# Optimization experiments

Hardware: AMD Instinct MI355X
Metric: run time of the kernel (lower is better)

## Reference

```python
import jax, jax.numpy as jnp
import numpy as np

N = 4096      # nnode
F = 128       # feature_dim
E = 64        # embed_dim
P_EDGE = 0.01 # edge probability (~41 avg degree)
NEG = -9e15
ALPHA = 0.2   # leaky relu slope


def _xavier(key, shape):
    lim = float(np.sqrt(6.0 / (shape[0] + shape[1])))
    return jax.random.uniform(key, shape, minval=-lim, maxval=lim, dtype=jnp.float32)


def setup_inputs() -> dict:
    key = jax.random.key(0)
    ks = jax.random.split(key, 14)
    features = jax.random.normal(ks[0], (N, F), dtype=jnp.float32)
    eye = jnp.eye(N, dtype=jnp.float32)

    def make_adj(k):
        a = (jax.random.uniform(k, (N, N)) < P_EDGE).astype(jnp.float32)
        return jnp.maximum(a, eye)  # self loop so no empty rows

    return {
        "features": features,
        "geo_adj": make_adj(ks[1]),
        "forward_adj": make_adj(ks[2]),
        "backward_adj": make_adj(ks[3]),
        "weight": _xavier(ks[4], (E, F)),
        "Wf": _xavier(ks[5], (F, E)),
        "af1": jax.random.normal(ks[6], (E,), dtype=jnp.float32) * 0.1,
        "af2": jax.random.normal(ks[7], (E,), dtype=jnp.float32) * 0.1,
        "Wb": _xavier(ks[8], (F, E)),
        "ab1": jax.random.normal(ks[9], (E,), dtype=jnp.float32) * 0.1,
        "ab2": jax.random.normal(ks[10], (E,), dtype=jnp.float32) * 0.1,
        "Wg": _xavier(ks[11], (F, E)),
        "ag1": jax.random.normal(ks[12], (E,), dtype=jnp.float32) * 0.1,
        "ag2": jax.random.normal(ks[13], (E,), dtype=jnp.float32) * 0.1,
    }


def _mean_neighbors(adj, feat):
    # pre_weight: row-normalized neighbor averaging, (N,N) @ (N,F)
    deg = jnp.clip(jnp.sum(adj, axis=1, keepdims=True), 1.0, None)
    return (adj @ feat) / deg


def _attention(feat, mask_feat, adj, W, a1, a2):
    # GAT-style additive attention with masked softmax over neighbors
    h = feat @ W        # (N, E)
    hm = mask_feat @ W  # (N, E)
    e = jax.nn.leaky_relu((h @ a1)[:, None] + (hm @ a2)[None, :], negative_slope=ALPHA)  # (N, N)
    e = jnp.where(adj > 0, e, NEG)
    return jax.nn.softmax(e, axis=1)  # (N, N)


def reference(features, geo_adj, forward_adj, backward_adj, weight,
              Wf, af1, af2, Wb, ab1, ab2, Wg, ag1, ag2):
    t = features  # (N, F)
    mask_f = _mean_neighbors(forward_adj, t)
    mask_b = _mean_neighbors(backward_adj, t)
    mask_g = _mean_neighbors(geo_adj, t)

    w_f = _attention(t, mask_f, forward_adj, Wf, af1, af2)
    w_b = _attention(t, mask_b, backward_adj, Wb, ab1, ab2)
    w_g = _attention(t, mask_g, geo_adj, Wg, ag1, ag2)

    # get_mask_matrix_i/_j broadcast-mul + sum(1) == attn @ t (or attn.T @ t)
    x = weight @ t.T                  # (E, N)
    x_fwd = weight @ (w_f @ t).T      # mask_matrix_i
    x_bwd = weight @ (w_b.T @ t).T    # mask_matrix_j (transposed)
    x_geo = weight @ (w_g @ t).T      # mask_matrix_i

    return jnp.concatenate([x, x_fwd, x_bwd, x_geo], axis=0)  # (4E, N)
```

## Files before the change

### kernel.cpp

```cpp
#include <hip/hip_runtime.h>

#define NN 4096
#define FF 128
#define EE 64

typedef unsigned short u16;

__device__ __forceinline__ float lrelu(float x) { return x > 0.f ? x : 0.2f * x; }

__global__ void k_prep(const float* __restrict__ Wf, const float* __restrict__ af1, const float* __restrict__ af2,
                       const float* __restrict__ Wb, const float* __restrict__ ab1, const float* __restrict__ ab2,
                       const float* __restrict__ Wg, const float* __restrict__ ag1, const float* __restrict__ ag2,
                       float* __restrict__ v6)
{
    const float* Ws[3]  = {Wf, Wb, Wg};
    const float* a1s[3] = {af1, ab1, ag1};
    const float* a2s[3] = {af2, ab2, ag2};
    int tid = threadIdx.x;
    for (int idx = tid; idx < 6 * FF; idx += 256) {
        int vi = idx >> 7, f = idx & (FF - 1), dd = vi >> 1;
        const float* a = (vi & 1) ? a2s[dd] : a1s[dd];
        const float* W = Ws[dd];
        float s = 0.f;
        for (int e = 0; e < EE; ++e) s += W[(size_t)f * EE + e] * a[e];
        v6[idx] = s;
    }
}

__global__ void k_feat(const float* __restrict__ t, const float* __restrict__ weight,
                       const float* __restrict__ v6,
                       float* __restrict__ u, float* __restrict__ s1, float* __restrict__ p,
                       float* __restrict__ out, int* __restrict__ ccnt)
{
    __shared__ __attribute__((aligned(16))) float tt[FF];
    __shared__ float vv[6 * FF];
    int n = blockIdx.x, tid = threadIdx.x;
    if (n < 16) ccnt[n * 256 + tid] = 0;
    if (tid < FF) tt[tid] = t[(size_t)n * FF + tid];
    for (int idx = tid; idx < 6 * FF; idx += 256) vv[idx] = v6[idx];
    __syncthreads();
    int e = tid >> 2, part = tid & 3;
    const float4* w4 = reinterpret_cast<const float4*>(weight + (size_t)e * FF + part * 32);
    const float4* t4 = reinterpret_cast<const float4*>(tt + part * 32);
    float s = 0.f;
    #pragma unroll
    for (int q8 = 0; q8 < 8; ++q8) {
        float4 w = w4[q8]; float4 x = t4[q8];
        s += w.x * x.x + w.y * x.y + w.z * x.z + w.w * x.w;
    }
    s += __shfl_xor(s, 1); s += __shfl_xor(s, 2);
    if (part == 0) {
        u[(size_t)n * EE + e] = s;
        out[(size_t)e * NN + n] = s;
    }
    if (tid < 64) {
        float t0 = tt[tid], t1 = tt[64 + tid];
        for (int vi = 0; vi < 6; ++vi) {
            float x = t0 * vv[vi * FF + tid] + t1 * vv[vi * FF + 64 + tid];
            for (int off = 32; off; off >>= 1) x += __shfl_xor(x, off);
            if (tid == 0) {
                int dd = vi >> 1;
                if (vi & 1) p[dd * NN + n] = x; else s1[dd * NN + n] = x;
            }
        }
    }
}

__global__ __launch_bounds__(256, 4)
void k_scan(const float* __restrict__ Af, const float* __restrict__ Ab, const float* __restrict__ Ag,
            const float* __restrict__ p,
            u16* __restrict__ csr, int* __restrict__ cnt, float* __restrict__ s2,
            u16* __restrict__ csc, int* __restrict__ ccnt, int stride)
{
    int wid = threadIdx.x >> 6, lane = threadIdx.x & 63;
    int gr = blockIdx.x * 4 + wid;
    int d = gr >> 12, r = gr & (NN - 1);
    const float* A = d == 0 ? Af : (d == 1 ? Ab : Ag);
    const float4* row4 = reinterpret_cast<const float4*>(A + (size_t)r * NN);
    const float* pd = p + d * NN;

    float4 l0 = row4[lane],        l1 = row4[64 + lane],  l2 = row4[128 + lane],
           l3 = row4[192 + lane],  l4 = row4[256 + lane], l5 = row4[320 + lane],
           l6 = row4[384 + lane],  l7 = row4[448 + lane], l8 = row4[512 + lane],
           l9 = row4[576 + lane],  l10 = row4[640 + lane], l11 = row4[704 + lane],
           l12 = row4[768 + lane], l13 = row4[832 + lane], l14 = row4[896 + lane],
           l15 = row4[960 + lane];

    unsigned long long mask = 0ull;
#define MBITS(L, J) { unsigned mm = (L.x != 0.f ? 1u : 0u) | (L.y != 0.f ? 2u : 0u) | \
                                    (L.z != 0.f ? 4u : 0u) | (L.w != 0.f ? 8u : 0u); \
                      mask |= ((unsigned long long)mm) << (J * 4); }
    MBITS(l0, 0)  MBITS(l1, 1)  MBITS(l2, 2)  MBITS(l3, 3)
    MBITS(l4, 4)  MBITS(l5, 5)  MBITS(l6, 6)  MBITS(l7, 7)
    MBITS(l8, 8)  MBITS(l9, 9)  MBITS(l10, 10) MBITS(l11, 11)
    MBITS(l12, 12) MBITS(l13, 13) MBITS(l14, 14) MBITS(l15, 15)
#undef MBITS

    int lc = __popcll(mask);
    int sc = lc;
    for (int off = 1; off < 64; off <<= 1) {
        int o = __shfl_up(sc, off);
        if (lane >= off) sc += o;
    }
    int total = __shfl(sc, 63);
    int pos = sc - lc;
    u16* crow = csr + (size_t)gr * stride;
    float q = 0.f;
    unsigned long long m = mask;
    while (m) {
        int b = __ffsll((unsigned long long)m) - 1;
        m &= m - 1;
        int col = ((b >> 2) << 8) + (lane << 2) + (b & 3);
        if (pos < stride) crow[pos] = (u16)col;
        pos++;
        q += pd[col];
        if (d == 1) {
            int cp = atomicAdd(&ccnt[col], 1);
            if (cp < stride) csc[(size_t)col * stride + cp] = (u16)r;
        }
    }
    for (int off = 32; off; off >>= 1) q += __shfl_xor(q, off);
    if (lane == 0) {
        cnt[gr] = total;
        s2[gr] = q / fmaxf((float)total, 1.f);
    }
}

__global__ void k_zb(const float* __restrict__ s1, const float* __restrict__ s2,
                     const u16* __restrict__ csr, const int* __restrict__ cnt, int stride,
                     float* __restrict__ Zb)
{
    int tid = threadIdx.x, wave = tid >> 6, lane = tid & 63;
    int j = blockIdx.x * 4 + wave;
    int gr = NN + j;
    int nnz = min(cnt[gr], stride);
    const u16* crow = csr + (size_t)gr * stride;
    float s1j = s1[gr];
    const float* s2b = s2 + NN;
    float z = 0.f;
    if (lane < nnz)      z += __expf(lrelu(s1j + s2b[crow[lane]]));
    if (lane + 64 < nnz) z += __expf(lrelu(s1j + s2b[crow[lane + 64]]));
    for (int off = 32; off; off >>= 1) z += __shfl_xor(z, off);
    if (lane == 0) Zb[j] = z;
}

__global__ void k_out(const float* __restrict__ u,
                      const float* __restrict__ s1, const float* __restrict__ s2,
                      const float* __restrict__ Zb,
                      const u16* __restrict__ csr, const int* __restrict__ cnt,
                      const u16* __restrict__ csc, const int* __restrict__ ccnt, int stride,
                      float* __restrict__ out)
{
    __shared__ float wl[128]; __shared__ int il[128];
    __shared__ float zsum; __shared__ float oacc[4 * EE];
    int gr = blockIdx.x;
    int d = gr >> 12, i = gr & (NN - 1);
    int tid = threadIdx.x, wave = tid >> 6, lane = tid & 63;
    if (tid == 0) zsum = 0.f;
    __syncthreads();
    float invz;
    int nnz;
    if (d == 1) {
        nnz = min(ccnt[i], stride);
        const u16* ccol = csc + (size_t)i * stride;
        float s2i = s2[NN + i];
        if (tid < nnz) {
            int j = ccol[tid];
            il[tid] = j;
            wl[tid] = __expf(lrelu(s1[NN + j] + s2i)) / Zb[j];
        }
        invz = 1.f;
        __syncthreads();
    } else {
        nnz = min(cnt[gr], stride);
        const u16* crow = csr + (size_t)gr * stride;
        float s1i = s1[gr];
        const float* s2d = s2 + d * NN;
        float z = 0.f;
        if (tid < nnz) {
            int col = crow[tid];
            float w = __expf(lrelu(s1i + s2d[col]));
            il[tid] = col; wl[tid] = w; z = w;
        }
        for (int off = 32; off; off >>= 1) z += __shfl_xor(z, off);
        if (lane == 0) atomicAdd(&zsum, z);
        __syncthreads();
        float zs = zsum;
        invz = zs > 0.f ? 1.f / zs : 0.f;
    }
    float a0 = 0.f, a1 = 0.f;
    int k = wave;
    for (; k + 4 < nnz; k += 8) {
        a0 += wl[k]     * u[(size_t)il[k]     * EE + lane];
        a1 += wl[k + 4] * u[(size_t)il[k + 4] * EE + lane];
    }
    for (; k < nnz; k += 4)
        a0 += wl[k] * u[(size_t)il[k] * EE + lane];
    oacc[wave * EE + lane] = a0 + a1;
    __syncthreads();
    if (wave == 0) {
        float rsum = (oacc[lane] + oacc[EE + lane] + oacc[2 * EE + lane] + oacc[3 * EE + lane]) * invz;
        int base = 64 + (d << 6);
        out[(size_t)(base + lane) * NN + i] = rsum;
    }
}

extern "C" void kernel_launch(void* const* d_in, const int* in_sizes, int n_in,
                              void* d_out, int out_size, void* d_ws, size_t ws_size,
                              hipStream_t stream)
{
    const float* t   = (const float*)d_in[0];
    const float* Ag  = (const float*)d_in[1];
    const float* Af  = (const float*)d_in[2];
    const float* Ab  = (const float*)d_in[3];
    const float* W   = (const float*)d_in[4];
    const float* Wf  = (const float*)d_in[5];
    const float* af1 = (const float*)d_in[6];
    const float* af2 = (const float*)d_in[7];
    const float* Wb  = (const float*)d_in[8];
    const float* ab1 = (const float*)d_in[9];
    const float* ab2 = (const float*)d_in[10];
    const float* Wg  = (const float*)d_in[11];
    const float* ag1 = (const float*)d_in[12];
    const float* ag2 = (const float*)d_in[13];
    float* out = (float*)d_out;

    float* ws = (float*)d_ws;
    float* v6  = ws;
    float* s1  = v6 + 6 * FF;
    float* p   = s1 + 3 * NN;
    float* s2  = p + 3 * NN;
    float* Zb  = s2 + 3 * NN;
    float* u   = Zb + NN;
    int*   cnt  = (int*)(u + (size_t)NN * EE);
    int*   ccnt = cnt + 3 * NN;
    u16*   csr  = (u16*)(ccnt + NN);

    size_t base_bytes = ((char*)csr) - ((char*)d_ws);
    int stride = 128;
    if (base_bytes + (size_t)4 * NN * 128 * 2 > ws_size) stride = 96;
    if (base_bytes + (size_t)4 * NN * 96 * 2 > ws_size)  stride = 64;
    u16* csc = csr + (size_t)3 * NN * stride;

    k_prep<<<1, 256, 0, stream>>>(Wf, af1, af2, Wb, ab1, ab2, Wg, ag1, ag2, v6);
    k_feat<<<NN, 256, 0, stream>>>(t, W, v6, u, s1, p, out, ccnt);
    k_scan<<<3 * NN / 4, 256, 0, stream>>>(Af, Ab, Ag, p, csr, cnt, s2, csc, ccnt, stride);
    k_zb<<<NN / 4, 256, 0, stream>>>(s1, s2, csr, cnt, stride, Zb);
    k_out<<<3 * NN, 256, 0, stream>>>(u, s1, s2, Zb, csr, cnt, csc, ccnt, stride, out);
}
```

Measured before the change: 278.6 us.

## Split adjacency scan into ballot-based bitmask kernel and separate CSR build kernel

The fused scan kernel becomes two kernels. The first streams the three dense adjacency matrices and packs nonzero flags into 64-bit ballot words, with no register-heavy sixteen-float4 preload and no long per-lane serial loop. The second reads the compact bitmasks and builds the CSR/CSC lists, row sums and counts. The aim is to let the bandwidth-bound pass over the 200MB of adjacency run at full occupancy, separated from the divergent atomic-heavy CSR construction. The cost is one extra launch and a 3MB mask round trip through memory.

```diff
diff --git a/kernel.cpp b/kernel.cpp
--- a/kernel.cpp
+++ b/kernel.cpp
@@ -5,6 +5,7 @@
 #define EE 64
 
 typedef unsigned short u16;
+typedef unsigned long long u64;
 
 __device__ __forceinline__ float lrelu(float x) { return x > 0.f ? x : 0.2f * x; }
 
@@ -66,37 +67,40 @@
     }
 }
 
-__global__ __launch_bounds__(256, 4)
-void k_scan(const float* __restrict__ Af, const float* __restrict__ Ab, const float* __restrict__ Ag,
-            const float* __restrict__ p,
-            u16* __restrict__ csr, int* __restrict__ cnt, float* __restrict__ s2,
-            u16* __restrict__ csc, int* __restrict__ ccnt, int stride)
+__global__ void k_mask(const float* __restrict__ Af, const float* __restrict__ Ab, const float* __restrict__ Ag,
+                       u64* __restrict__ masks)
 {
     int wid = threadIdx.x >> 6, lane = threadIdx.x & 63;
     int gr = blockIdx.x * 4 + wid;
     int d = gr >> 12, r = gr & (NN - 1);
     const float* A = d == 0 ? Af : (d == 1 ? Ab : Ag);
     const float4* row4 = reinterpret_cast<const float4*>(A + (size_t)r * NN);
-    const float* pd = p + d * NN;
-
-    float4 l0 = row4[lane],        l1 = row4[64 + lane],  l2 = row4[128 + lane],
-           l3 = row4[192 + lane],  l4 = row4[256 + lane], l5 = row4[320 + lane],
-           l6 = row4[384 + lane],  l7 = row4[448 + lane], l8 = row4[512 + lane],
-           l9 = row4[576 + lane],  l10 = row4[640 + lane], l11 = row4[704 + lane],
-           l12 = row4[768 + lane], l13 = row4[832 + lane], l14 = row4[896 + lane],
-           l15 = row4[960 + lane];
-
-    unsigned long long mask = 0ull;
-#define MBITS(L, J) { unsigned mm = (L.x != 0.f ? 1u : 0u) | (L.y != 0.f ? 2u : 0u) | \
-                                    (L.z != 0.f ? 4u : 0u) | (L.w != 0.f ? 8u : 0u); \
-                      mask |= ((unsigned long long)mm) << (J * 4); }
-    MBITS(l0, 0)  MBITS(l1, 1)  MBITS(l2, 2)  MBITS(l3, 3)
-    MBITS(l4, 4)  MBITS(l5, 5)  MBITS(l6, 6)  MBITS(l7, 7)
-    MBITS(l8, 8)  MBITS(l9, 9)  MBITS(l10, 10) MBITS(l11, 11)
-    MBITS(l12, 12) MBITS(l13, 13) MBITS(l14, 14) MBITS(l15, 15)
-#undef MBITS
-
-    int lc = __popcll(mask);
+    u64 w = 0ull;
+    #pragma unroll
+    for (int j = 0; j < 16; ++j) {
+        float4 L = row4[j * 64 + lane];
+        u64 bx = __ballot(L.x != 0.f);
+        u64 by = __ballot(L.y != 0.f);
+        u64 bz = __ballot(L.z != 0.f);
+        u64 bw = __ballot(L.w != 0.f);
+        int base = j * 4;
+        if (lane == base)     w = bx;
+        if (lane == base + 1) w = by;
+        if (lane == base + 2) w = bz;
+        if (lane == base + 3) w = bw;
+    }
+    masks[(size_t)gr * 64 + lane] = w;
+}
+
+__global__ void k_csr(const u64* __restrict__ masks, const float* __restrict__ p,
+                      u16* __restrict__ csr, int* __restrict__ cnt, float* __restrict__ s2,
+                      u16* __restrict__ csc, int* __restrict__ ccnt, int stride)
+{
+    int wid = threadIdx.x >> 6, lane = threadIdx.x & 63;
+    int gr = blockIdx.x * 4 + wid;
+    int d = gr >> 12, r = gr & (NN - 1);
+    u64 m = masks[(size_t)gr * 64 + lane];
+    int lc = __popcll(m);
     int sc = lc;
     for (int off = 1; off < 64; off <<= 1) {
         int o = __shfl_up(sc, off);
@@ -104,13 +108,14 @@
     }
     int total = __shfl(sc, 63);
     int pos = sc - lc;
+    const float* pd = p + d * NN;
     u16* crow = csr + (size_t)gr * stride;
+    int colbase = (lane >> 2) * 256 + (lane & 3);
     float q = 0.f;
-    unsigned long long m = mask;
     while (m) {
-        int b = __ffsll((unsigned long long)m) - 1;
+        int b = __ffsll(m) - 1;
         m &= m - 1;
-        int col = ((b >> 2) << 8) + (lane << 2) + (b & 3);
+        int col = colbase + b * 4;
         if (pos < stride) crow[pos] = (u16)col;
         pos++;
         q += pd[col];
@@ -225,8 +230,9 @@
     const float* ag2 = (const float*)d_in[13];
     float* out = (float*)d_out;
 
-    float* ws = (float*)d_ws;
-    float* v6  = ws;
+    char* wsb = (char*)d_ws;
+    u64*   masks = (u64*)wsb;
+    float* v6  = (float*)(wsb + (size_t)3 * NN * 64 * 8);
     float* s1  = v6 + 6 * FF;
     float* p   = s1 + 3 * NN;
     float* s2  = p + 3 * NN;
@@ -236,7 +242,7 @@
     int*   ccnt = cnt + 3 * NN;
     u16*   csr  = (u16*)(ccnt + NN);
 
-    size_t base_bytes = ((char*)csr) - ((char*)d_ws);
+    size_t base_bytes = ((char*)csr) - wsb;
     int stride = 128;
     if (base_bytes + (size_t)4 * NN * 128 * 2 > ws_size) stride = 96;
     if (base_bytes + (size_t)4 * NN * 96 * 2 > ws_size)  stride = 64;
@@ -244,7 +250,8 @@
 
     k_prep<<<1, 256, 0, stream>>>(Wf, af1, af2, Wb, ab1, ab2, Wg, ag1, ag2, v6);
     k_feat<<<NN, 256, 0, stream>>>(t, W, v6, u, s1, p, out, ccnt);
-    k_scan<<<3 * NN / 4, 256, 0, stream>>>(Af, Ab, Ag, p, csr, cnt, s2, csc, ccnt, stride);
+    k_mask<<<3 * NN / 4, 256, 0, stream>>>(Af, Ab, Ag, masks);
+    k_csr<<<3 * NN / 4, 256, 0, stream>>>(masks, p, csr, cnt, s2, csc, ccnt, stride);
     k_zb<<<NN / 4, 256, 0, stream>>>(s1, s2, csr, cnt, stride, Zb);
     k_out<<<3 * NN, 256, 0, stream>>>(u, s1, s2, Zb, csr, cnt, csc, ccnt, stride, out);
 }
```

Result: slower. 298.7 us (+7.2%).

## Fuse attention-vector prep into feature kernel and make scan grid-stride

Applied to the files above, without the earlier changes.

Removes the single-block prep kernel by having every k_feat block compute the six W·a projection vectors directly into shared memory, which saves one launch but repeats that small computation in each of the 4096 blocks. The scan kernel moves to a persistent 1024-block grid-stride loop with its row loads rolled into an unrolled loop, which changes how many row loads are in flight. In k_out, the shared-memory atomic for the softmax denominator becomes a per-wave reduction, and normalisation is applied to the weights before accumulation.

```diff
diff --git a/kernel.cpp b/kernel.cpp
--- a/kernel.cpp
+++ b/kernel.cpp
@@ -5,39 +5,34 @@
 #define EE 64
 
 typedef unsigned short u16;
+typedef unsigned long long u64;
 
 __device__ __forceinline__ float lrelu(float x) { return x > 0.f ? x : 0.2f * x; }
 
-__global__ void k_prep(const float* __restrict__ Wf, const float* __restrict__ af1, const float* __restrict__ af2,
+__global__ void k_feat(const float* __restrict__ t, const float* __restrict__ weight,
+                       const float* __restrict__ Wf, const float* __restrict__ af1, const float* __restrict__ af2,
                        const float* __restrict__ Wb, const float* __restrict__ ab1, const float* __restrict__ ab2,
                        const float* __restrict__ Wg, const float* __restrict__ ag1, const float* __restrict__ ag2,
-                       float* __restrict__ v6)
-{
+                       float* __restrict__ u, float* __restrict__ s1, float* __restrict__ p,
+                       float* __restrict__ out, int* __restrict__ ccnt)
+{
+    __shared__ __attribute__((aligned(16))) float tt[FF];
+    __shared__ float vv[6 * FF];
     const float* Ws[3]  = {Wf, Wb, Wg};
     const float* a1s[3] = {af1, ab1, ag1};
     const float* a2s[3] = {af2, ab2, ag2};
-    int tid = threadIdx.x;
+    int n = blockIdx.x, tid = threadIdx.x;
+    if (n < 16) ccnt[n * 256 + tid] = 0;
+    if (tid < FF) tt[tid] = t[(size_t)n * FF + tid];
     for (int idx = tid; idx < 6 * FF; idx += 256) {
         int vi = idx >> 7, f = idx & (FF - 1), dd = vi >> 1;
         const float* a = (vi & 1) ? a2s[dd] : a1s[dd];
-        const float* W = Ws[dd];
+        const float* W = Ws[dd] + (size_t)f * EE;
         float s = 0.f;
-        for (int e = 0; e < EE; ++e) s += W[(size_t)f * EE + e] * a[e];
-        v6[idx] = s;
-    }
-}
-
-__global__ void k_feat(const float* __restrict__ t, const float* __restrict__ weight,
-                       const float* __restrict__ v6,
-                       float* __restrict__ u, float* __restrict__ s1, float* __restrict__ p,
-                       float* __restrict__ out, int* __restrict__ ccnt)
-{
-    __shared__ __attribute__((aligned(16))) float tt[FF];
-    __shared__ float vv[6 * FF];
-    int n = blockIdx.x, tid = threadIdx.x;
-    if (n < 16) ccnt[n * 256 + tid] = 0;
-    if (tid < FF) tt[tid] = t[(size_t)n * FF + tid];
-    for (int idx = tid; idx < 6 * FF; idx += 256) vv[idx] = v6[idx];
+        #pragma unroll 8
+        for (int e = 0; e < EE; ++e) s += W[e] * a[e];
+        vv[idx] = s;
+    }
     __syncthreads();
     int e = tid >> 2, part = tid & 3;
     const float4* w4 = reinterpret_cast<const float4*>(weight + (size_t)e * FF + part * 32);
@@ -73,56 +68,50 @@
             u16* __restrict__ csc, int* __restrict__ ccnt, int stride)
 {
     int wid = threadIdx.x >> 6, lane = threadIdx.x & 63;
-    int gr = blockIdx.x * 4 + wid;
-    int d = gr >> 12, r = gr & (NN - 1);
-    const float* A = d == 0 ? Af : (d == 1 ? Ab : Ag);
-    const float4* row4 = reinterpret_cast<const float4*>(A + (size_t)r * NN);
-    const float* pd = p + d * NN;
-
-    float4 l0 = row4[lane],        l1 = row4[64 + lane],  l2 = row4[128 + lane],
-           l3 = row4[192 + lane],  l4 = row4[256 + lane], l5 = row4[320 + lane],
-           l6 = row4[384 + lane],  l7 = row4[448 + lane], l8 = row4[512 + lane],
-           l9 = row4[576 + lane],  l10 = row4[640 + lane], l11 = row4[704 + lane],
-           l12 = row4[768 + lane], l13 = row4[832 + lane], l14 = row4[896 + lane],
-           l15 = row4[960 + lane];
-
-    unsigned long long mask = 0ull;
-#define MBITS(L, J) { unsigned mm = (L.x != 0.f ? 1u : 0u) | (L.y != 0.f ? 2u : 0u) | \
-                                    (L.z != 0.f ? 4u : 0u) | (L.w != 0.f ? 8u : 0u); \
-                      mask |= ((unsigned long long)mm) << (J * 4); }
-    MBITS(l0, 0)  MBITS(l1, 1)  MBITS(l2, 2)  MBITS(l3, 3)
-    MBITS(l4, 4)  MBITS(l5, 5)  MBITS(l6, 6)  MBITS(l7, 7)
-    MBITS(l8, 8)  MBITS(l9, 9)  MBITS(l10, 10) MBITS(l11, 11)
-    MBITS(l12, 12) MBITS(l13, 13) MBITS(l14, 14) MBITS(l15, 15)
-#undef MBITS
-
-    int lc = __popcll(mask);
-    int sc = lc;
-    for (int off = 1; off < 64; off <<= 1) {
-        int o = __shfl_up(sc, off);
-        if (lane >= off) sc += o;
-    }
-    int total = __shfl(sc, 63);
-    int pos = sc - lc;
-    u16* crow = csr + (size_t)gr * stride;
-    float q = 0.f;
-    unsigned long long m = mask;
-    while (m) {
-        int b = __ffsll((unsigned long long)m) - 1;
-        m &= m - 1;
-        int col = ((b >> 2) << 8) + (lane << 2) + (b & 3);
-        if (pos < stride) crow[pos] = (u16)col;
-        pos++;
-        q += pd[col];
-        if (d == 1) {
-            int cp = atomicAdd(&ccnt[col], 1);
-            if (cp < stride) csc[(size_t)col * stride + cp] = (u16)r;
-        }
-    }
-    for (int off = 32; off; off >>= 1) q += __shfl_xor(q, off);
-    if (lane == 0) {
-        cnt[gr] = total;
-        s2[gr] = q / fmaxf((float)total, 1.f);
+    int wv = blockIdx.x * 4 + wid;
+    for (int gr = wv; gr < 3 * NN; gr += 4096) {
+        int d = gr >> 12, r = gr & (NN - 1);
+        const float* A = d == 0 ? Af : (d == 1 ? Ab : Ag);
+        const float4* row4 = reinterpret_cast<const float4*>(A + (size_t)r * NN);
+        const float* pd = p + d * NN;
+
+        u64 mask = 0ull;
+        #pragma unroll
+        for (int j = 0; j < 16; ++j) {
+            float4 L = row4[j * 64 + lane];
+            unsigned mm = (L.x != 0.f ? 1u : 0u) | (L.y != 0.f ? 2u : 0u) |
+                          (L.z != 0.f ? 4u : 0u) | (L.w != 0.f ? 8u : 0u);
+            mask |= ((u64)mm) << (j * 4);
+        }
+
+        int lc = __popcll(mask);
+        int sc = lc;
+        for (int off = 1; off < 64; off <<= 1) {
+            int o = __shfl_up(sc, off);
+            if (lane >= off) sc += o;
+        }
+        int total = __shfl(sc, 63);
+        int pos = sc - lc;
+        u16* crow = csr + (size_t)gr * stride;
+        float q = 0.f;
+        u64 m = mask;
+        while (m) {
+            int b = __ffsll(m) - 1;
+            m &= m - 1;
+            int col = ((b >> 2) << 8) + (lane << 2) + (b & 3);
+            if (pos < stride) crow[pos] = (u16)col;
+            pos++;
+            q += pd[col];
+            if (d == 1) {
+                int cp = atomicAdd(&ccnt[col], 1);
+                if (cp < stride) csc[(size_t)col * stride + cp] = (u16)r;
+            }
+        }
+        for (int off = 32; off; off >>= 1) q += __shfl_xor(q, off);
+        if (lane == 0) {
+            cnt[gr] = total;
+            s2[gr] = q / fmaxf((float)total, 1.f);
+        }
     }
 }
 
@@ -152,24 +141,20 @@
                       float* __restrict__ out)
 {
     __shared__ float wl[128]; __shared__ int il[128];
-    __shared__ float zsum; __shared__ float oacc[4 * EE];
+    __shared__ float zred[4]; __shared__ float oacc[4 * EE];
     int gr = blockIdx.x;
     int d = gr >> 12, i = gr & (NN - 1);
     int tid = threadIdx.x, wave = tid >> 6, lane = tid & 63;
-    if (tid == 0) zsum = 0.f;
-    __syncthreads();
-    float invz;
     int nnz;
     if (d == 1) {
         nnz = min(ccnt[i], stride);
-        const u16* ccol = csc + (size_t)i * stride;
+        const u16* cc = csc + (size_t)i * stride;
         float s2i = s2[NN + i];
         if (tid < nnz) {
-            int j = ccol[tid];
+            int j = cc[tid];
             il[tid] = j;
             wl[tid] = __expf(lrelu(s1[NN + j] + s2i)) / Zb[j];
         }
-        invz = 1.f;
         __syncthreads();
     } else {
         nnz = min(cnt[gr], stride);
@@ -178,15 +163,17 @@
         const float* s2d = s2 + d * NN;
         float z = 0.f;
         if (tid < nnz) {
-            int col = crow[tid];
-            float w = __expf(lrelu(s1i + s2d[col]));
-            il[tid] = col; wl[tid] = w; z = w;
+            int c = crow[tid];
+            float w = __expf(lrelu(s1i + s2d[c]));
+            il[tid] = c; wl[tid] = w; z = w;
         }
         for (int off = 32; off; off >>= 1) z += __shfl_xor(z, off);
-        if (lane == 0) atomicAdd(&zsum, z);
+        if (lane == 0) zred[wave] = z;
         __syncthreads();
-        float zs = zsum;
-        invz = zs > 0.f ? 1.f / zs : 0.f;
+        float invz = zred[0] + zred[1] + zred[2] + zred[3];
+        invz = invz > 0.f ? 1.f / invz : 0.f;
+        if (tid < nnz) wl[tid] *= invz;
+        __syncthreads();
     }
     float a0 = 0.f, a1 = 0.f;
     int k = wave;
@@ -199,7 +186,7 @@
     oacc[wave * EE + lane] = a0 + a1;
     __syncthreads();
     if (wave == 0) {
-        float rsum = (oacc[lane] + oacc[EE + lane] + oacc[2 * EE + lane] + oacc[3 * EE + lane]) * invz;
+        float rsum = oacc[lane] + oacc[EE + lane] + oacc[2 * EE + lane] + oacc[3 * EE + lane];
         int base = 64 + (d << 6);
         out[(size_t)(base + lane) * NN + i] = rsum;
     }
@@ -226,8 +213,7 @@
     float* out = (float*)d_out;
 
     float* ws = (float*)d_ws;
-    float* v6  = ws;
-    float* s1  = v6 + 6 * FF;
+    float* s1  = ws;
     float* p   = s1 + 3 * NN;
     float* s2  = p + 3 * NN;
     float* Zb  = s2 + 3 * NN;
@@ -242,9 +228,9 @@
     if (base_bytes + (size_t)4 * NN * 96 * 2 > ws_size)  stride = 64;
     u16* csc = csr + (size_t)3 * NN * stride;
 
-    k_prep<<<1, 256, 0, stream>>>(Wf, af1, af2, Wb, ab1, ab2, Wg, ag1, ag2, v6);
-    k_feat<<<NN, 256, 0, stream>>>(t, W, v6, u, s1, p, out, ccnt);
-    k_scan<<<3 * NN / 4, 256, 0, stream>>>(Af, Ab, Ag, p, csr, cnt, s2, csc, ccnt, stride);
+    k_feat<<<NN, 256, 0, stream>>>(t, W, Wf, af1, af2, Wb, ab1, ab2, Wg, ag1, ag2,
+                                   u, s1, p, out, ccnt);
+    k_scan<<<1024, 256, 0, stream>>>(Af, Ab, Ag, p, csr, cnt, s2, csc, ccnt, stride);
     k_zb<<<NN / 4, 256, 0, stream>>>(s1, s2, csr, cnt, stride, Zb);
     k_out<<<3 * NN, 256, 0, stream>>>(u, s1, s2, Zb, csr, cnt, csc, ccnt, stride, out);
 }
```

New measurement: 388.7 us. 39.5% more time.
